# Performance work log

Measured on AMD Instinct MI355X. Metric: run time of the kernel, lower is better.

## Reference

```python
import jax, jax.numpy as jnp
import numpy as np

B, P, LD, TD = 4096, 10, 512, 512  # batch, num_max_paths, lane_feat_dim, traj_enc_h_dim
DIN = 2 * LD + 2 * TD


def setup_inputs() -> dict:
    key = jax.random.key(0)
    ks = jax.random.split(key, 7)
    agent_context = jax.random.normal(ks[0], (B, TD), jnp.float32)
    lane_contexts = jax.random.normal(ks[1], (B, P, LD), jnp.float32)
    ngh_lane_context = jax.random.normal(ks[2], (B, P, LD), jnp.float32)
    ngh_contexts = jax.random.normal(ks[3], (B, P, TD), jnp.float32)
    # lane_label must be one-hot per row (argwhere(label==1) in the original)
    idx = jax.random.randint(ks[4], (B,), 0, P)
    lane_label = jax.nn.one_hot(idx, P, dtype=jnp.int32)
    W1 = jax.random.normal(ks[5], (DIN, LD), jnp.float32) / np.sqrt(DIN).astype(np.float32)
    b1 = jnp.zeros((LD,), jnp.float32)
    W2 = jax.random.normal(ks[6], (LD * P, P), jnp.float32) / np.sqrt(LD * P).astype(np.float32)
    b2 = jnp.zeros((P,), jnp.float32)
    return {
        "agent_context": agent_context,
        "lane_contexts": lane_contexts,
        "ngh_lane_context": ngh_lane_context,
        "ngh_contexts": ngh_contexts,
        "lane_label": lane_label,
        "W1": W1, "b1": b1, "W2": W2, "b2": b2,
    }


def reference(agent_context, lane_contexts, ngh_lane_context, ngh_contexts,
              lane_label, W1, b1, W2, b2):
    b, p = lane_contexts.shape[:2]
    # agent_context repeated over the path dim, then concat on feature dim
    agent_rep = jnp.broadcast_to(agent_context[:, None, :], (b, p, agent_context.shape[-1]))
    ctx = jnp.concatenate([agent_rep, lane_contexts, ngh_lane_context, ngh_contexts], axis=2)  # [B,P,DIN]
    emb = jax.nn.relu(jnp.einsum('bpd,de->bpe', ctx, W1) + b1)  # [B,P,LD]
    logits = emb.reshape(b, -1) @ W2 + b2  # [B,P]
    # vectorized replacement of the per-batch argwhere loop: first index where label==1
    idx = jnp.argmax(lane_label, axis=1)  # [B]
    rows = jnp.arange(b)
    best_lane_contexts = lane_contexts[rows, idx]        # [B,LD]
    best_ngh_lane_contexts = ngh_lane_context[rows, idx]  # [B,LD]
    best_ngh_contexts = ngh_contexts[rows, idx]           # [B,TD]
    return logits, best_lane_contexts, best_ngh_lane_contexts, best_ngh_contexts
```

## Files before the change

### kernel.cpp

```cpp
#include <hip/hip_runtime.h>

typedef __attribute__((ext_vector_type(4))) float f32x4;
typedef __attribute__((ext_vector_type(8))) short short8;
typedef __attribute__((ext_vector_type(4))) short short4v;
typedef __attribute__((ext_vector_type(8))) unsigned short ushort8;

__device__ __forceinline__ unsigned short f2bf(float f) {
  unsigned u = __float_as_uint(f);
  u = (u + 0x7fffu + ((u >> 16) & 1u)) >> 16;
  return (unsigned short)u;
}
__device__ __forceinline__ float bf2f(unsigned short h) {
  return __uint_as_float(((unsigned)h) << 16);
}

__global__ __launch_bounds__(256) void prep_w1_k(const float* __restrict__ W1,
                                                 unsigned short* __restrict__ W1t2) {
  int f = blockIdx.x * 256 + threadIdx.x;
  int kt = f >> 14;
  int r = f & 16383;
  int n = r >> 5;
  int kk = r & 31;
  W1t2[f] = f2bf(W1[(kt * 32 + kk) * 512 + n]);
}

__global__ __launch_bounds__(256) void prep_w2_k(const float* __restrict__ W2,
                                                 unsigned short* __restrict__ W2t) {
  int f = blockIdx.x * 256 + threadIdx.x;
  int j = f / 5120;
  int k = f - j * 5120;
  W2t[f] = f2bf(W2[k * 10 + j]);
}

__global__ __launch_bounds__(512) void gemm1_k(
    const float* __restrict__ agent, const float* __restrict__ lanec,
    const float* __restrict__ nghl, const float* __restrict__ nghc,
    const unsigned short* __restrict__ W1t2, const float* __restrict__ b1,
    unsigned short* __restrict__ emb)
{
  __shared__ __align__(16) short Alds[2][64][40];
  const int tid = threadIdx.x;
  const int wid = tid >> 6;
  const int lane = tid & 63;
  const int m0 = blockIdx.x * 64;

  const int srow = tid >> 3;
  const int scol = (tid & 7) << 2;
  const int mrow = m0 + srow;
  const int rowoff = mrow * 512 + scol;
  const int rowoff_a = (mrow / 10) * 512 + scol;

  const int fr = lane & 15;
  const int fk = (lane >> 4) << 3;

  const unsigned short* Bbase = W1t2 + (wid * 64 + fr) * 32 + fk;

  auto loadA = [&](int kt) -> f32x4 {
    int k0 = kt << 5;
    const float* p;
    if (k0 < 512)       p = agent + rowoff_a + k0;
    else if (k0 < 1024) p = lanec + rowoff + (k0 - 512);
    else if (k0 < 1536) p = nghl  + rowoff + (k0 - 1024);
    else                p = nghc  + rowoff + (k0 - 1536);
    return *(const f32x4*)p;
  };

  f32x4 acc[4][4];
  #pragma unroll
  for (int i = 0; i < 4; ++i)
    #pragma unroll
    for (int j = 0; j < 4; ++j) acc[i][j] = (f32x4)0.f;

  {
    f32x4 v = loadA(0);
    short4v w;
    #pragma unroll
    for (int i = 0; i < 4; ++i) w[i] = (short)f2bf(v[i]);
    *(short4v*)&Alds[0][srow][scol] = w;
  }
  f32x4 pf0 = loadA(1);
  f32x4 pf1 = loadA(2);
  short8 bpre[4];
  #pragma unroll
  for (int ni = 0; ni < 4; ++ni) bpre[ni] = *(const short8*)(Bbase + ni * 512);

  int cur = 0;
  for (int kt = 0; kt < 64; ++kt) {
    __syncthreads();
    short8 af[4];
    #pragma unroll
    for (int mi = 0; mi < 4; ++mi)
      af[mi] = *(const short8*)&Alds[cur][mi * 16 + fr][fk];
    short8 bc[4];
    #pragma unroll
    for (int ni = 0; ni < 4; ++ni) bc[ni] = bpre[ni];
    if (kt < 63) {
      const unsigned short* bp = Bbase + (kt + 1) * 16384;
      #pragma unroll
      for (int ni = 0; ni < 4; ++ni) bpre[ni] = *(const short8*)(bp + ni * 512);
    }
    f32x4 wv = pf0;
    pf0 = pf1;
    if (kt < 61) pf1 = loadA(kt + 3);
    #pragma unroll
    for (int mi = 0; mi < 4; ++mi)
      #pragma unroll
      for (int ni = 0; ni < 4; ++ni)
        acc[mi][ni] = __builtin_amdgcn_mfma_f32_16x16x32_bf16(af[mi], bc[ni], acc[mi][ni], 0, 0, 0);
    if (kt < 63) {
      short4v w;
      #pragma unroll
      for (int i = 0; i < 4; ++i) w[i] = (short)f2bf(wv[i]);
      *(short4v*)&Alds[cur ^ 1][srow][scol] = w;
    }
    cur ^= 1;
  }

  float b1v[4];
  #pragma unroll
  for (int ni = 0; ni < 4; ++ni) b1v[ni] = b1[wid * 64 + ni * 16 + fr];
  const int r0 = (lane >> 4) << 2;
  #pragma unroll
  for (int mi = 0; mi < 4; ++mi) {
    #pragma unroll
    for (int r = 0; r < 4; ++r) {
      int m = m0 + mi * 16 + r0 + r;
      unsigned short* erow = emb + m * 512 + wid * 64 + fr;
      #pragma unroll
      for (int ni = 0; ni < 4; ++ni) {
        float v = acc[mi][ni][r] + b1v[ni];
        v = fmaxf(v, 0.f);
        erow[ni * 16] = f2bf(v);
      }
    }
  }
}

__global__ __launch_bounds__(256) void logits_k(
    const unsigned short* __restrict__ emb, const unsigned short* __restrict__ W2t,
    const float* __restrict__ b2, float* __restrict__ out)
{
  int b = (blockIdx.x * 256 + threadIdx.x) >> 6;
  int lane = threadIdx.x & 63;
  float acc[10];
  #pragma unroll
  for (int j = 0; j < 10; ++j) acc[j] = 0.f;
  const unsigned short* erow = emb + b * 5120 + lane * 8;
  const unsigned short* wbase = W2t + lane * 8;
  #pragma unroll
  for (int i = 0; i < 10; ++i) {
    ushort8 ev = *(const ushort8*)(erow + i * 512);
    float ef[8];
    #pragma unroll
    for (int t = 0; t < 8; ++t) ef[t] = bf2f(ev[t]);
    #pragma unroll
    for (int j = 0; j < 10; ++j) {
      ushort8 wv = *(const ushort8*)(wbase + j * 5120 + i * 512);
      #pragma unroll
      for (int t = 0; t < 8; ++t) acc[j] = fmaf(ef[t], bf2f(wv[t]), acc[j]);
    }
  }
  #pragma unroll
  for (int j = 0; j < 10; ++j)
    #pragma unroll
    for (int m = 1; m < 64; m <<= 1) acc[j] += __shfl_xor(acc[j], m, 64);
  if (lane == 0) {
    #pragma unroll
    for (int j = 0; j < 10; ++j) out[b * 10 + j] = acc[j] + b2[j];
  }
}

__global__ __launch_bounds__(384) void gather_k(
    const float* __restrict__ lanec, const float* __restrict__ nghl,
    const float* __restrict__ nghc, const int* __restrict__ label,
    float* __restrict__ out)
{
  int b = blockIdx.x;
  const int* lb = label + b * 10;
  int idx = 0;
  #pragma unroll
  for (int j = 9; j >= 0; --j) if (lb[j] == 1) idx = j;
  int g = threadIdx.x >> 7;
  int i = (threadIdx.x & 127) << 2;
  const float* src = (g == 0 ? lanec : (g == 1 ? nghl : nghc)) + (b * 10 + idx) * 512 + i;
  float* dst = out + (g == 0 ? 40960 : (g == 1 ? 2138112 : 4235264)) + b * 512 + i;
  *(f32x4*)dst = *(const f32x4*)src;
}

extern "C" void kernel_launch(void* const* d_in, const int* in_sizes, int n_in,
                              void* d_out, int out_size, void* d_ws, size_t ws_size,
                              hipStream_t stream) {
  const float* agent = (const float*)d_in[0];
  const float* lanec = (const float*)d_in[1];
  const float* nghl  = (const float*)d_in[2];
  const float* nghc  = (const float*)d_in[3];
  const int*   label = (const int*)d_in[4];
  const float* W1    = (const float*)d_in[5];
  const float* b1    = (const float*)d_in[6];
  const float* W2    = (const float*)d_in[7];
  const float* b2    = (const float*)d_in[8];
  float* out = (float*)d_out;

  unsigned short* emb  = (unsigned short*)d_ws;
  unsigned short* W1t2 = (unsigned short*)((char*)d_ws + 41943040);
  unsigned short* W2t  = (unsigned short*)((char*)d_ws + 41943040 + 2097152);

  prep_w1_k<<<4096, 256, 0, stream>>>(W1, W1t2);
  prep_w2_k<<<200, 256, 0, stream>>>(W2, W2t);
  gemm1_k<<<640, 512, 0, stream>>>(agent, lanec, nghl, nghc, W1t2, b1, emb);
  logits_k<<<1024, 256, 0, stream>>>(emb, W2t, b2, out);
  gather_k<<<4096, 384, 0, stream>>>(lanec, nghl, nghc, label, out);
}
```

Before: 450.1 us.

## Coalesce weight prep, deepen A prefetch, relax barrier, split gather index

prep_w1_k now transposes W1 through shared memory in tiles and issues vector loads and stores instead of strided scalar accesses. prep_w2_k now reads W2 coalesced and scatters its writes. In gemm1_k the A prefetch grows to three stages, the launch bounds request 4 waves per SIMD, and __syncthreads becomes a raw lgkmcnt wait plus s_barrier. The label argmax moves into a separate idx_k kernel whose result the flattened gather kernel reads. The new index buffer lives at the start of the workspace, which aliases emb, but it is written after logits_k has consumed emb, so stream ordering keeps this safe.

```diff
diff --git a/kernel.cpp b/kernel.cpp
--- a/kernel.cpp
+++ b/kernel.cpp
@@ -16,23 +16,44 @@
 
 __global__ __launch_bounds__(256) void prep_w1_k(const float* __restrict__ W1,
                                                  unsigned short* __restrict__ W1t2) {
-  int f = blockIdx.x * 256 + threadIdx.x;
-  int kt = f >> 14;
-  int r = f & 16383;
-  int n = r >> 5;
-  int kk = r & 31;
-  W1t2[f] = f2bf(W1[(kt * 32 + kk) * 512 + n]);
+  __shared__ short Lt[32][136];
+  const int t = threadIdx.x;
+  const int kt = blockIdx.x >> 2;
+  const int nq = blockIdx.x & 3;
+  #pragma unroll
+  for (int p = 0; p < 4; ++p) {
+    int idx = p * 256 + t;
+    int row = idx >> 5;
+    int c4 = idx & 31;
+    f32x4 v = *(const f32x4*)&W1[(kt * 32 + row) * 512 + nq * 128 + c4 * 4];
+    short4v w;
+    #pragma unroll
+    for (int i = 0; i < 4; ++i) w[i] = (short)f2bf(v[i]);
+    *(short4v*)&Lt[row][c4 * 4] = w;
+  }
+  __syncthreads();
+  unsigned short* obase = W1t2 + kt * 16384 + nq * 4096;
+  #pragma unroll
+  for (int q = 0; q < 2; ++q) {
+    int g = q * 2048 + t * 8;
+    int n_l = g >> 5;
+    int kk0 = g & 31;
+    short8 s;
+    #pragma unroll
+    for (int j = 0; j < 8; ++j) s[j] = Lt[kk0 + j][n_l];
+    *(short8*)&obase[g] = s;
+  }
 }
 
 __global__ __launch_bounds__(256) void prep_w2_k(const float* __restrict__ W2,
                                                  unsigned short* __restrict__ W2t) {
   int f = blockIdx.x * 256 + threadIdx.x;
-  int j = f / 5120;
-  int k = f - j * 5120;
-  W2t[f] = f2bf(W2[k * 10 + j]);
-}
-
-__global__ __launch_bounds__(512) void gemm1_k(
+  int k = f / 10;
+  int j = f - k * 10;
+  W2t[j * 5120 + k] = f2bf(W2[f]);
+}
+
+__global__ __launch_bounds__(512, 4) void gemm1_k(
     const float* __restrict__ agent, const float* __restrict__ lanec,
     const float* __restrict__ nghl, const float* __restrict__ nghc,
     const unsigned short* __restrict__ W1t2, const float* __restrict__ b1,
@@ -80,28 +101,30 @@
   }
   f32x4 pf0 = loadA(1);
   f32x4 pf1 = loadA(2);
-  short8 bpre[4];
-  #pragma unroll
-  for (int ni = 0; ni < 4; ++ni) bpre[ni] = *(const short8*)(Bbase + ni * 512);
+  f32x4 pf2 = loadA(3);
+  short8 bq[4];
+  #pragma unroll
+  for (int ni = 0; ni < 4; ++ni) bq[ni] = *(const short8*)(Bbase + ni * 512);
 
   int cur = 0;
   for (int kt = 0; kt < 64; ++kt) {
-    __syncthreads();
+    asm volatile("s_waitcnt lgkmcnt(0)\n\ts_barrier" ::: "memory");
     short8 af[4];
     #pragma unroll
     for (int mi = 0; mi < 4; ++mi)
       af[mi] = *(const short8*)&Alds[cur][mi * 16 + fr][fk];
     short8 bc[4];
     #pragma unroll
-    for (int ni = 0; ni < 4; ++ni) bc[ni] = bpre[ni];
+    for (int ni = 0; ni < 4; ++ni) bc[ni] = bq[ni];
     if (kt < 63) {
       const unsigned short* bp = Bbase + (kt + 1) * 16384;
       #pragma unroll
-      for (int ni = 0; ni < 4; ++ni) bpre[ni] = *(const short8*)(bp + ni * 512);
+      for (int ni = 0; ni < 4; ++ni) bq[ni] = *(const short8*)(bp + ni * 512);
     }
     f32x4 wv = pf0;
     pf0 = pf1;
-    if (kt < 61) pf1 = loadA(kt + 3);
+    pf1 = pf2;
+    if (kt < 60) pf2 = loadA(kt + 4);
     #pragma unroll
     for (int mi = 0; mi < 4; ++mi)
       #pragma unroll
@@ -170,20 +193,31 @@
   }
 }
 
-__global__ __launch_bounds__(384) void gather_k(
+__global__ __launch_bounds__(256) void idx_k(const int* __restrict__ label,
+                                             int* __restrict__ idxbuf) {
+  int b = blockIdx.x * 256 + threadIdx.x;
+  if (b < 4096) {
+    const int* lb = label + b * 10;
+    int idx = 0;
+    #pragma unroll
+    for (int j = 9; j >= 0; --j) if (lb[j] == 1) idx = j;
+    idxbuf[b] = idx;
+  }
+}
+
+__global__ __launch_bounds__(256) void gather_k(
     const float* __restrict__ lanec, const float* __restrict__ nghl,
-    const float* __restrict__ nghc, const int* __restrict__ label,
+    const float* __restrict__ nghc, const int* __restrict__ idxbuf,
     float* __restrict__ out)
 {
-  int b = blockIdx.x;
-  const int* lb = label + b * 10;
-  int idx = 0;
-  #pragma unroll
-  for (int j = 9; j >= 0; --j) if (lb[j] == 1) idx = j;
-  int g = threadIdx.x >> 7;
-  int i = (threadIdx.x & 127) << 2;
-  const float* src = (g == 0 ? lanec : (g == 1 ? nghl : nghc)) + (b * 10 + idx) * 512 + i;
-  float* dst = out + (g == 0 ? 40960 : (g == 1 ? 2138112 : 4235264)) + b * 512 + i;
+  int g = blockIdx.x * 256 + threadIdx.x;
+  int t = g >> 19;
+  int r = g & 524287;
+  int b = r >> 7;
+  int i = (r & 127) << 2;
+  int idx = idxbuf[b];
+  const float* src = (t == 0 ? lanec : (t == 1 ? nghl : nghc)) + (b * 10 + idx) * 512 + i;
+  float* dst = out + (t == 0 ? 40960 : (t == 1 ? 2138112 : 4235264)) + b * 512 + i;
   *(f32x4*)dst = *(const f32x4*)src;
 }
 
@@ -204,10 +238,12 @@
   unsigned short* emb  = (unsigned short*)d_ws;
   unsigned short* W1t2 = (unsigned short*)((char*)d_ws + 41943040);
   unsigned short* W2t  = (unsigned short*)((char*)d_ws + 41943040 + 2097152);
-
-  prep_w1_k<<<4096, 256, 0, stream>>>(W1, W1t2);
+  int* idxbuf = (int*)d_ws;
+
+  prep_w1_k<<<256, 256, 0, stream>>>(W1, W1t2);
   prep_w2_k<<<200, 256, 0, stream>>>(W2, W2t);
   gemm1_k<<<640, 512, 0, stream>>>(agent, lanec, nghl, nghc, W1t2, b1, emb);
   logits_k<<<1024, 256, 0, stream>>>(emb, W2t, b2, out);
-  gather_k<<<4096, 384, 0, stream>>>(lanec, nghl, nghc, label, out);
-}
+  idx_k<<<16, 256, 0, stream>>>(label, idxbuf);
+  gather_k<<<6144, 256, 0, stream>>>(lanec, nghl, nghc, idxbuf, out);
+}
```

New measurement: 511.0 us. +13.5%, slower.
